# Kernel tuning notes

Measured on AMD Instinct MI355X. Metric: run time of the kernel, lower is better.

The kernel has to match this reference:

```python
import jax, jax.numpy as jnp
import numpy as np

HIDDEN = 768
FF = 3072
N_HEADS = 12
HEAD = HIDDEN // N_HEADS
WIDTH = 512  # attention window (number of attended keys, causal)
B, S = 2, 4096
EPS = 1e-6


def _rotary_sincos(seq_len, dim):
    # GPT-J style: freqs per pair, each value repeated twice (interleaved)
    inv_freq = 1.0 / (10000.0 ** (np.arange(0, dim, 2, dtype=np.float32) / dim))
    t = np.arange(seq_len, dtype=np.float32)
    ang = np.einsum('s,d->sd', t, inv_freq)              # [S, dim/2]
    ang = np.repeat(ang, 2, axis=-1)                     # [S, dim]
    return jnp.asarray(np.sin(ang))[:, None, :], jnp.asarray(np.cos(ang))[:, None, :]


def setup_inputs() -> dict:
    key = jax.random.key(0)
    ks = jax.random.split(key, 4)
    x = jax.random.normal(ks[0], (B, S, HIDDEN), dtype=jnp.float32)
    sin, cos = _rotary_sincos(S, HEAD)                   # [S,1,HEAD] each
    W_in = jax.random.normal(ks[1], (HIDDEN, 3 * HIDDEN + FF), dtype=jnp.float32) / np.sqrt(HIDDEN)
    b_in = jnp.zeros((3 * HIDDEN + FF,), dtype=jnp.float32)
    W_out = jax.random.normal(ks[2], (HIDDEN + FF, HIDDEN), dtype=jnp.float32) / np.sqrt(HIDDEN + FF)
    b_out = jnp.zeros((HIDDEN,), dtype=jnp.float32)
    w_norm = jnp.ones((HIDDEN,), dtype=jnp.float32)
    return {"x": x, "sin": sin, "cos": cos, "w_norm": w_norm,
            "W_in": W_in, "b_in": b_in, "W_out": W_out, "b_out": b_out}


def _rotate_every_two(x):
    x1 = x[..., ::2]
    x2 = x[..., 1::2]
    return jnp.stack((-x2, x1), axis=-1).reshape(x.shape)


def _apply_rope(x, sin, cos):
    # x: [B,S,H,hd]; sin/cos: [S,1,hd] -> broadcast as [1,S,1,hd]
    sin = sin[None]
    cos = cos[None]
    return x * cos + _rotate_every_two(x) * sin


def _windowed_attention(q, k, v, width):
    # q,k,v: [B,S,H,hd]; causal local attention: key j valid iff 0 <= i-j < width
    b, s, h, d = q.shape
    wb = width  # block size == window; each query block attends blocks (b-1, b)
    nb = s // wb
    scale = 1.0 / np.sqrt(d)
    qb = q.reshape(b, nb, wb, h, d)
    kp = jnp.pad(k, ((0, 0), (wb, 0), (0, 0), (0, 0))).reshape(b, nb + 1, wb, h, d)
    vp = jnp.pad(v, ((0, 0), (wb, 0), (0, 0), (0, 0))).reshape(b, nb + 1, wb, h, d)
    kb = jnp.concatenate([kp[:, :-1], kp[:, 1:]], axis=2)   # [B,nb,2wb,H,hd]
    vb = jnp.concatenate([vp[:, :-1], vp[:, 1:]], axis=2)
    scores = jnp.einsum('bnqhd,bnkhd->bnhqk', qb, kb) * scale
    qi = jnp.arange(wb)
    ki = jnp.arange(2 * wb)
    bi = jnp.arange(nb)
    diff = wb + qi[:, None] - ki[None, :]                    # i - j per block
    base = (diff >= 0) & (diff < width)                      # [wb, 2wb]
    valid_j = (bi[:, None, None] >= 1) | (ki[None, None, :] >= wb)  # j >= 0
    mask = base[None] & valid_j                              # [nb, wb, 2wb]
    neg = jnp.finfo(scores.dtype).min
    scores = jnp.where(mask[None, :, None], scores, neg)
    p = jax.nn.softmax(scores, axis=-1)
    out = jnp.einsum('bnhqk,bnkhd->bnqhd', p, vb)
    return out.reshape(b, s, h * d)


def reference(x, sin, cos, w_norm, W_in, b_in, W_out, b_out):
    # RMSNorm
    ms = jnp.mean(x * x, axis=-1, keepdims=True)
    xn = x * jax.lax.rsqrt(ms + EPS) * w_norm
    # fused QKV + FF projection
    t = xn @ W_in + b_in                                     # [B,S,3*HIDDEN+FF]
    ff = t[:, :, -FF:]
    qkv = t[:, :, :-FF].reshape(x.shape[0], x.shape[1], 3, N_HEADS, HEAD)
    q = _apply_rope(qkv[:, :, 0], sin, cos)
    k = _apply_rope(qkv[:, :, 1], sin, cos)
    v = qkv[:, :, 2]
    attn = _windowed_attention(q, k, v, WIDTH)               # [B,S,HIDDEN]
    ff = jax.nn.gelu(ff, approximate=False)
    combined = jnp.concatenate((attn, ff), axis=-1)          # [B,S,HIDDEN+FF]
    return combined @ W_out + b_out
```

## Files before the change

kernel.cpp:

```cpp
#include <hip/hip_runtime.h>
#include <hip/hip_bf16.h>

typedef short bf16x8 __attribute__((ext_vector_type(8)));
typedef float f32x4 __attribute__((ext_vector_type(4)));

#define LOG2E 1.4426950408889634f
#define QKV_E ((size_t)24*4096*64)

__device__ __forceinline__ float bfu2f(unsigned short u) {
  unsigned v = ((unsigned)u) << 16;
  return __builtin_bit_cast(float, v);
}
__device__ __forceinline__ unsigned short f2bfu(float f) {
  unsigned u = __builtin_bit_cast(unsigned, f);
  u += 0x7fffu + ((u >> 16) & 1u);
  return (unsigned short)(u >> 16);
}
__device__ __forceinline__ unsigned packbf2(float lo, float hi) {
  return (unsigned)f2bfu(lo) | ((unsigned)f2bfu(hi) << 16);
}
__device__ __forceinline__ float gelu_f(float v) {
  float a = fabsf(v) * 0.70710678118654752f;
  float t = 1.0f / (1.0f + 0.3275911f * a);
  float poly = ((((1.061405429f * t - 1.453152027f) * t + 1.421413741f) * t
                 - 0.284496736f) * t + 0.254829592f) * t;
  float erfa = 1.0f - poly * __expf(-a * a);
  float erfv = v >= 0.0f ? erfa : -erfa;
  return 0.5f * v * (1.0f + erfv);
}
__device__ __forceinline__ void gl_lds16(const ushort* g, ushort* l) {
  __builtin_amdgcn_global_load_lds(
      (const __attribute__((address_space(1))) unsigned int*)(const void*)g,
      (__attribute__((address_space(3))) unsigned int*)(void*)l, 16, 0, 0);
}
#define WAIT_VM8  asm volatile("s_waitcnt vmcnt(8)" ::: "memory")
#define WAIT_VM2  asm volatile("s_waitcnt vmcnt(2)" ::: "memory")
#define WAIT_VM0  asm volatile("s_waitcnt vmcnt(0)" ::: "memory")
#define WAIT_LGKM asm volatile("s_waitcnt lgkmcnt(0)" ::: "memory")
#define BAR       __builtin_amdgcn_s_barrier()

__global__ __launch_bounds__(256) void rmsnorm_k(const float* __restrict__ x,
    const float* __restrict__ w, ushort* __restrict__ xn) {
  int row = blockIdx.x, t = threadIdx.x;
  const float* xr = x + (size_t)row * 768;
  float v0 = xr[t], v1 = xr[t + 256], v2 = xr[t + 512];
  float ss = v0 * v0 + v1 * v1 + v2 * v2;
#pragma unroll
  for (int m = 32; m >= 1; m >>= 1) ss += __shfl_xor(ss, m, 64);
  __shared__ float part[4];
  if ((t & 63) == 0) part[t >> 6] = ss;
  __syncthreads();
  float tot = part[0] + part[1] + part[2] + part[3];
  float rr = rsqrtf(tot * (1.0f / 768.0f) + 1e-6f);
  ushort* xo = xn + (size_t)row * 768;
  xo[t]       = f2bfu(v0 * rr * w[t]);
  xo[t + 256] = f2bfu(v1 * rr * w[t + 256]);
  xo[t + 512] = f2bfu(v2 * rr * w[t + 512]);
}

__global__ __launch_bounds__(256) void tcvt_k(const float* __restrict__ in,
    ushort* __restrict__ out, int R, int C) {
  __shared__ float tile[32][33];
  int c0 = blockIdx.x * 32, r0 = blockIdx.y * 32;
  int t = threadIdx.x;
  int j = t & 31, i0 = t >> 5;
#pragma unroll
  for (int i = i0; i < 32; i += 8) tile[i][j] = in[(size_t)(r0 + i) * C + c0 + j];
  __syncthreads();
#pragma unroll
  for (int i = i0; i < 32; i += 8) out[(size_t)(c0 + i) * R + r0 + j] = f2bfu(tile[j][i]);
}

__global__ __launch_bounds__(512, 2) void gemm1_k(const ushort* __restrict__ A,
    const ushort* __restrict__ Bt, const float* __restrict__ bias,
    const float* __restrict__ sn, const float* __restrict__ cs,
    ushort* __restrict__ qbuf, ushort* __restrict__ kbuf,
    ushort* __restrict__ vt, ushort* __restrict__ comb) {
  __shared__ __align__(16) ushort lds[2][32768];
  const int t = threadIdx.x, lane = t & 63, w = t >> 6;
  const int wm = w >> 2, wn = w & 3;
  const int g = lane >> 4, q15 = lane & 15;
  int bid = blockIdx.x;
  int xcd = bid & 7, local = bid >> 3;
  int grp = local / 28, r28 = local % 28;
  int bx = grp * 7 + r28 % 7;
  int by = xcd * 4 + r28 / 7;
  const int mBase = by * 256, nBase = bx * 256;

  const int schk = ((t & 7) ^ ((t >> 3) & 7)) * 8;
  const ushort* gA = A  + (size_t)(mBase + (t >> 3)) * 768 + schk;
  const ushort* gB = Bt + (size_t)(nBase + (t >> 3)) * 768 + schk;
  const int dstBase = w * 512;

  f32x4 acc[8][4];
  f32x4 z = {0.f, 0.f, 0.f, 0.f};
#pragma unroll
  for (int mi = 0; mi < 8; ++mi)
#pragma unroll
    for (int nj = 0; nj < 4; ++nj) acc[mi][nj] = z;

#pragma unroll
  for (int rd = 0; rd < 4; ++rd) {
    gl_lds16(gB + rd * 49152, &lds[0][16384 + rd * 4096 + dstBase]);
    gl_lds16(gA + rd * 49152, &lds[0][rd * 4096 + dstBase]);
  }
  WAIT_VM0;
  BAR;

#pragma unroll 1
  for (int kt = 0; kt < 12; ++kt) {
    const int cur = kt & 1;
    const ushort* As = &lds[cur][0];
    const ushort* Bs = &lds[cur][16384];
    ushort* nb = &lds[1 - cur][0];
    bf16x8 bff[4];
#pragma unroll
    for (int p = 0; p < 4; ++p) {
      if (kt < 11) {
        const int k1 = (kt + 1) * 64;
        if (p == 0) {
          gl_lds16(gB + k1,               nb + 16384 + dstBase);
          gl_lds16(gB + 49152 + k1,       nb + 16384 + 4096 + dstBase);
        } else if (p == 1) {
          gl_lds16(gB + 2 * 49152 + k1,   nb + 16384 + 2 * 4096 + dstBase);
          gl_lds16(gB + 3 * 49152 + k1,   nb + 16384 + 3 * 4096 + dstBase);
        } else if (p == 2) {
          gl_lds16(gA + k1,               nb + dstBase);
          gl_lds16(gA + 2 * 49152 + k1,   nb + 2 * 4096 + dstBase);
        } else {
          gl_lds16(gA + 49152 + k1,       nb + 4096 + dstBase);
          gl_lds16(gA + 3 * 49152 + k1,   nb + 3 * 4096 + dstBase);
        }
      }
      const int kk = p >> 1, mih = p & 1;
      const int slot = ((kk * 4 + g) ^ (q15 & 7)) << 3;
      if (mih == 0) {
#pragma unroll
        for (int nj = 0; nj < 4; ++nj)
          bff[nj] = *(const bf16x8*)(Bs + (wn * 64 + nj * 16 + q15) * 64 + slot);
      }
      bf16x8 af[4];
#pragma unroll
      for (int i = 0; i < 4; ++i)
        af[i] = *(const bf16x8*)(As + (wm * 128 + (mih * 4 + i) * 16 + q15) * 64 + slot);
      BAR;
      WAIT_LGKM;
      __builtin_amdgcn_sched_barrier(0);
      __builtin_amdgcn_s_setprio(1);
#pragma unroll
      for (int i = 0; i < 4; ++i)
#pragma unroll
        for (int nj = 0; nj < 4; ++nj)
          acc[mih * 4 + i][nj] = __builtin_amdgcn_mfma_f32_16x16x32_bf16(
              bff[nj], af[i], acc[mih * 4 + i][nj], 0, 0, 0);
      __builtin_amdgcn_s_setprio(0);
      if (kt < 11) { WAIT_VM2; } else { WAIT_VM0; }
      BAR;
    }
  }

  const int colB = nBase + wn * 64;
  const bool isff = (colB >= 2304);
  const int region = colB / 768;
#pragma unroll
  for (int mi = 0; mi < 8; ++mi) {
    int row = mBase + wm * 128 + mi * 16 + q15;
    int b = row >> 12, s = row & 4095;
#pragma unroll
    for (int nj = 0; nj < 4; ++nj) {
      int col = colB + nj * 16 + g * 4;
      f32x4 v = acc[mi][nj] + *(const f32x4*)(bias + col);
      if (isff) {
        ushort4 o;
        o.x = f2bfu(gelu_f(v[0]));
        o.y = f2bfu(gelu_f(v[1]));
        o.z = f2bfu(gelu_f(v[2]));
        o.w = f2bfu(gelu_f(v[3]));
        *(ushort4*)(comb + (size_t)row * 3840 + (col - 1536)) = o;
      } else {
        int rem = col - region * 768;
        int h = rem >> 6, d0 = rem & 63;
        if (region == 2) {
          int l = s & 127;
          int pnn = l >> 4, pg = (l >> 2) & 3, pr = l & 3;
          int sp = (s & ~127) | (((pnn >> 1) * 4 + pg) * 8 + (pnn & 1) * 4 + pr);
          size_t vb = (size_t)((b * 12 + h) * 64 + d0) * 4096 + sp;
          vt[vb]          = f2bfu(v[0]);
          vt[vb + 4096]   = f2bfu(v[1]);
          vt[vb + 2*4096] = f2bfu(v[2]);
          vt[vb + 3*4096] = f2bfu(v[3]);
        } else {
          f32x4 sv = *(const f32x4*)(sn + (s << 6) + d0);
          f32x4 cv = *(const f32x4*)(cs + (s << 6) + d0);
          float o0 = v[0] * cv[0] - v[1] * sv[0];
          float o1 = v[1] * cv[0] + v[0] * sv[0];
          float o2 = v[2] * cv[2] - v[3] * sv[2];
          float o3 = v[3] * cv[2] + v[2] * sv[2];
          ushort4 o;
          if (region == 0) {
            o.x = f2bfu(o0 * 0.125f); o.y = f2bfu(o1 * 0.125f);
            o.z = f2bfu(o2 * 0.125f); o.w = f2bfu(o3 * 0.125f);
            *(ushort4*)(qbuf + ((size_t)((b * 12 + h) * 4096 + s)) * 64 + d0) = o;
          } else {
            o.x = f2bfu(o0); o.y = f2bfu(o1); o.z = f2bfu(o2); o.w = f2bfu(o3);
            *(ushort4*)(kbuf + ((size_t)((b * 12 + h) * 4096 + s)) * 64 + d0) = o;
          }
        }
      }
    }
  }
}

__global__ __launch_bounds__(256, 2) void gemm2_k(const ushort* __restrict__ A,
    const ushort* __restrict__ Bt, const float* __restrict__ bias,
    float* __restrict__ out) {
  __shared__ __align__(16) ushort lds[2][2][128 * 64];
  const int t = threadIdx.x, lane = t & 63, w = t >> 6;
  const int wr = w >> 1, wc = w & 1;
  int bid = blockIdx.x;
  int xcd = bid & 7, local = bid >> 3;
  int g = local / 4, r4 = local % 4;
  int bx = (g % 3) * 2 + (r4 & 1);
  int by = xcd * 8 + (g / 3) * 2 + (r4 >> 1);
  const int mBase = by * 128, nBase = bx * 128;

  size_t gA[4], gB[4];
  int ldst[4];
#pragma unroll
  for (int j = 0; j < 4; ++j) {
    int row = w * 32 + j * 8 + (lane >> 3);
    int gc = ((lane & 7) ^ (lane >> 3)) * 8;
    gA[j] = (size_t)(mBase + row) * 3840 + gc;
    gB[j] = (size_t)(nBase + row) * 3840 + gc;
    ldst[j] = (w * 32 + j * 8) * 64;
  }

  f32x4 acc[4][4];
  f32x4 z = {0.f, 0.f, 0.f, 0.f};
#pragma unroll
  for (int m = 0; m < 4; ++m)
#pragma unroll
    for (int nn = 0; nn < 4; ++nn) acc[m][nn] = z;

#pragma unroll
  for (int j = 0; j < 4; ++j) {
    gl_lds16(A + gA[j], &lds[0][0][0] + ldst[j]);
    gl_lds16(Bt + gB[j], &lds[0][1][0] + ldst[j]);
  }

#pragma unroll 1
  for (int kt = 0; kt < 60; ++kt) {
    const int cur = kt & 1;
    if (kt < 59) {
      int k0 = (kt + 1) * 64;
#pragma unroll
      for (int j = 0; j < 4; ++j) {
        gl_lds16(A + gA[j] + k0, &lds[1 - cur][0][0] + ldst[j]);
        gl_lds16(Bt + gB[j] + k0, &lds[1 - cur][1][0] + ldst[j]);
      }
      WAIT_VM8;
    } else {
      WAIT_VM0;
    }
    BAR;
    const ushort* As = &lds[cur][0][0];
    const ushort* Bs = &lds[cur][1][0];
#pragma unroll
    for (int kk = 0; kk < 2; ++kk) {
      bf16x8 af[4], bff[4];
#pragma unroll
      for (int m = 0; m < 4; ++m) {
        int row = wr * 64 + m * 16 + (lane & 15);
        int slot = (kk * 4 + (lane >> 4)) ^ (lane & 7);
        af[m] = *(const bf16x8*)(As + row * 64 + slot * 8);
      }
#pragma unroll
      for (int nn = 0; nn < 4; ++nn) {
        int row = wc * 64 + nn * 16 + (lane & 15);
        int slot = (kk * 4 + (lane >> 4)) ^ (lane & 7);
        bff[nn] = *(const bf16x8*)(Bs + row * 64 + slot * 8);
      }
#pragma unroll
      for (int m = 0; m < 4; ++m)
#pragma unroll
        for (int nn = 0; nn < 4; ++nn)
          acc[m][nn] = __builtin_amdgcn_mfma_f32_16x16x32_bf16(bff[nn], af[m], acc[m][nn], 0, 0, 0);
    }
    WAIT_LGKM;
    BAR;
  }

#pragma unroll
  for (int m = 0; m < 4; ++m) {
    int row = mBase + wr * 64 + m * 16 + (lane & 15);
#pragma unroll
    for (int nn = 0; nn < 4; ++nn) {
      int col = nBase + wc * 64 + nn * 16 + ((lane >> 4) << 2);
      f32x4 v = acc[m][nn] + *(const f32x4*)(bias + col);
      *(f32x4*)(out + (size_t)row * 768 + col) = v;
    }
  }
}

__global__ __launch_bounds__(256, 2) void attn_k(const ushort* __restrict__ qb,
    const ushort* __restrict__ kb, const ushort* __restrict__ vt,
    ushort* __restrict__ comb) {
  __shared__ __align__(16) ushort KS[2][128 * 64];
  __shared__ __align__(16) ushort VS[2][64 * 128];
  int bid = blockIdx.x;
  int nb = (bid & 7) * 96 + (bid >> 3);
  int qt = nb & 31, bh = nb >> 5;
  const int t = threadIdx.x, lane = t & 63, w = t >> 6;
  const int g = lane >> 4, q15 = lane & 15;
  const int qlo = qt * 128;
  const size_t base = (size_t)bh * 4096 * 64;

  size_t kSrc[4], vSrc[4];
  int dstOff[4];
#pragma unroll
  for (int j = 0; j < 4; ++j) {
    int ck = (w * 4 + j) * 64 + lane;
    int key = ck >> 3, sl = ck & 7;
    kSrc[j] = (size_t)key * 64 + ((sl ^ (key & 7)) << 3);
    int dd = ck >> 4, s16 = ck & 15;
    vSrc[j] = (size_t)dd * 4096 + ((s16 ^ (dd & 15)) << 3);
    dstOff[j] = (w * 4 + j) * 512;
  }

  bf16x8 qa[2][2];
#pragma unroll
  for (int m = 0; m < 2; ++m)
#pragma unroll
    for (int kk = 0; kk < 2; ++kk) {
      int row = qlo + w * 32 + m * 16 + q15;
      qa[m][kk] = *(const bf16x8*)(qb + base + (size_t)row * 64 + kk * 32 + g * 8);
    }

  f32x4 z = {0.f, 0.f, 0.f, 0.f};
  f32x4 o[2][4];
#pragma unroll
  for (int m = 0; m < 2; ++m)
#pragma unroll
    for (int df = 0; df < 4; ++df) o[m][df] = z;
  float m_run[2] = {-1e30f, -1e30f}, l_run[2] = {0.f, 0.f};

  const int t0 = qt >= 4 ? qt - 4 : 0;
  const int nt = qt - t0 + 1;
  {
    int k0 = t0 * 128;
#pragma unroll
    for (int j = 0; j < 4; ++j) {
      gl_lds16(kb + base + (size_t)k0 * 64 + kSrc[j], &KS[0][0] + dstOff[j]);
      gl_lds16(vt + base + k0 + vSrc[j], &VS[0][0] + dstOff[j]);
    }
  }

  const int qrow0 = qlo + w * 32 + q15;
#pragma unroll 1
  for (int it = 0; it < nt; ++it) {
    const int kt = t0 + it, k0 = kt * 128, cur = it & 1;
    if (it + 1 < nt) {
      int k1 = k0 + 128;
#pragma unroll
      for (int j = 0; j < 4; ++j) {
        gl_lds16(kb + base + (size_t)k1 * 64 + kSrc[j], &KS[1 - cur][0] + dstOff[j]);
        gl_lds16(vt + base + k1 + vSrc[j], &VS[1 - cur][0] + dstOff[j]);
      }
      WAIT_VM8;
    } else {
      WAIT_VM0;
    }
    BAR;
    f32x4 s[2][8];
#pragma unroll
    for (int m = 0; m < 2; ++m)
#pragma unroll
      for (int nn = 0; nn < 8; ++nn) s[m][nn] = z;
#pragma unroll
    for (int kk = 0; kk < 2; ++kk) {
      bf16x8 kf[8];
#pragma unroll
      for (int nn = 0; nn < 8; ++nn) {
        int row = nn * 16 + q15;
        int slot = (kk * 4 + g) ^ (q15 & 7);
        kf[nn] = *(const bf16x8*)(&KS[cur][0] + row * 64 + slot * 8);
      }
#pragma unroll
      for (int m = 0; m < 2; ++m)
#pragma unroll
        for (int nn = 0; nn < 8; ++nn)
          s[m][nn] = __builtin_amdgcn_mfma_f32_16x16x32_bf16(kf[nn], qa[m][kk], s[m][nn], 0, 0, 0);
    }
    if (kt == qt) {
#pragma unroll
      for (int m = 0; m < 2; ++m) {
        int ql = qrow0 + m * 16 - k0;
#pragma unroll
        for (int nn = 0; nn < 8; ++nn)
#pragma unroll
          for (int r = 0; r < 4; ++r)
            if (nn * 16 + g * 4 + r > ql) s[m][nn][r] = -3e38f;
      }
    } else if (kt == qt - 4) {
#pragma unroll
      for (int m = 0; m < 2; ++m) {
        int ql = qrow0 + m * 16 - k0;
#pragma unroll
        for (int nn = 0; nn < 8; ++nn)
#pragma unroll
          for (int r = 0; r < 4; ++r)
            if (ql - (nn * 16 + g * 4 + r) >= 512) s[m][nn][r] = -3e38f;
      }
    }
    float mx[2];
    bool need = false;
#pragma unroll
    for (int m = 0; m < 2; ++m) {
      float v = s[m][0][0];
#pragma unroll
      for (int nn = 0; nn < 8; ++nn)
#pragma unroll
        for (int r = 0; r < 4; ++r) v = fmaxf(v, s[m][nn][r]);
      v = fmaxf(v, __shfl_xor(v, 16, 64));
      v = fmaxf(v, __shfl_xor(v, 32, 64));
      mx[m] = v;
      need |= (v > m_run[m] + 8.f);
    }
    if (__any(need)) {
#pragma unroll
      for (int m = 0; m < 2; ++m) {
        float mn = fmaxf(m_run[m], mx[m]);
        float sc = exp2f((m_run[m] - mn) * LOG2E);
        m_run[m] = mn;
        l_run[m] *= sc;
#pragma unroll
        for (int df = 0; df < 4; ++df) o[m][df] *= sc;
      }
    }
#pragma unroll
    for (int m = 0; m < 2; ++m) {
      float mr = m_run[m];
      float ls = 0.f;
#pragma unroll
      for (int nn = 0; nn < 8; ++nn)
#pragma unroll
        for (int r = 0; r < 4; ++r) {
          float p = exp2f((s[m][nn][r] - mr) * LOG2E);
          s[m][nn][r] = p;
          ls += p;
        }
      ls += __shfl_xor(ls, 16, 64);
      ls += __shfl_xor(ls, 32, 64);
      l_run[m] += ls;
    }
#pragma unroll
    for (int kk2 = 0; kk2 < 4; ++kk2) {
      bf16x8 pa[2];
#pragma unroll
      for (int m = 0; m < 2; ++m) {
        int4 pi4;
        pi4.x = (int)packbf2(s[m][2*kk2][0],   s[m][2*kk2][1]);
        pi4.y = (int)packbf2(s[m][2*kk2][2],   s[m][2*kk2][3]);
        pi4.z = (int)packbf2(s[m][2*kk2+1][0], s[m][2*kk2+1][1]);
        pi4.w = (int)packbf2(s[m][2*kk2+1][2], s[m][2*kk2+1][3]);
        pa[m] = __builtin_bit_cast(bf16x8, pi4);
      }
#pragma unroll
      for (int df = 0; df < 4; ++df) {
        int row = df * 16 + q15;
        int slot = (kk2 * 4 + g) ^ q15;
        bf16x8 vf = *(const bf16x8*)(&VS[cur][0] + row * 128 + slot * 8);
#pragma unroll
        for (int m = 0; m < 2; ++m)
          o[m][df] = __builtin_amdgcn_mfma_f32_16x16x32_bf16(vf, pa[m], o[m][df], 0, 0, 0);
      }
    }
    WAIT_LGKM;
    BAR;
  }

  int b = bh / 12, h = bh % 12;
#pragma unroll
  for (int m = 0; m < 2; ++m) {
    float inv = 1.0f / l_run[m];
    int row = qrow0 + m * 16;
#pragma unroll
    for (int df = 0; df < 4; ++df) {
      ushort4 ov;
      ov.x = f2bfu(o[m][df][0] * inv);
      ov.y = f2bfu(o[m][df][1] * inv);
      ov.z = f2bfu(o[m][df][2] * inv);
      ov.w = f2bfu(o[m][df][3] * inv);
      *(ushort4*)(comb + (size_t)(b * 4096 + row) * 3840 + h * 64 + df * 16 + g * 4) = ov;
    }
  }
}

extern "C" void kernel_launch(void* const* d_in, const int* in_sizes, int n_in,
                              void* d_out, int out_size, void* d_ws, size_t ws_size,
                              hipStream_t stream) {
  (void)in_sizes; (void)n_in; (void)out_size; (void)ws_size;
  const float* x      = (const float*)d_in[0];
  const float* sin_t  = (const float*)d_in[1];
  const float* cos_t  = (const float*)d_in[2];
  const float* w_norm = (const float*)d_in[3];
  const float* W_in   = (const float*)d_in[4];
  const float* b_in   = (const float*)d_in[5];
  const float* W_out  = (const float*)d_in[6];
  const float* b_out  = (const float*)d_in[7];
  float* out = (float*)d_out;

  const size_t XN_E  = (size_t)8192 * 768;
  ushort* xn      = (ushort*)d_ws;
  ushort* qbuf    = xn + XN_E;
  ushort* kbuf    = qbuf + QKV_E;
  ushort* vt      = kbuf + QKV_E;
  ushort* w_in_t  = vt + QKV_E;
  ushort* w_out_t = w_in_t + (size_t)5376 * 768;
  ushort* comb    = w_out_t + (size_t)768 * 3840;

  rmsnorm_k<<<dim3(8192), dim3(256), 0, stream>>>(x, w_norm, xn);
  tcvt_k<<<dim3(5376 / 32, 768 / 32), dim3(256), 0, stream>>>(W_in, w_in_t, 768, 5376);
  tcvt_k<<<dim3(768 / 32, 3840 / 32), dim3(256), 0, stream>>>(W_out, w_out_t, 3840, 768);
  gemm1_k<<<dim3(672), dim3(512), 0, stream>>>(xn, w_in_t, b_in, sin_t, cos_t,
                                               qbuf, kbuf, vt, comb);
  attn_k<<<dim3(768), dim3(256), 0, stream>>>(qbuf, kbuf, vt, comb);
  gemm2_k<<<dim3(384), dim3(256), 0, stream>>>(comb, w_out_t, b_out, out);
}
```

Baseline: 239.4 us.

## Split-K gemm2 across two warp groups and simplify gemm1 pipeline

gemm2 now runs 512 threads per block, and each half of the block handles one half of the K dimension. The two partial accumulators are summed through LDS before the bias add and store, which doubles the waves per output tile to improve latency hiding. In exchange, gemm2 loses its double-buffered prefetch: every K step does a load followed by two __syncthreads with no overlap. gemm1's main loop is also restructured from four interleaved sub-phases, each with its own barriers and setprio, into a single prefetch-then-compute step per K tile with one wait and barrier.

```diff
diff --git a/kernel.cpp b/kernel.cpp
--- a/kernel.cpp
+++ b/kernel.cpp
@@ -34,7 +34,6 @@
       (__attribute__((address_space(3))) unsigned int*)(void*)l, 16, 0, 0);
 }
 #define WAIT_VM8  asm volatile("s_waitcnt vmcnt(8)" ::: "memory")
-#define WAIT_VM2  asm volatile("s_waitcnt vmcnt(2)" ::: "memory")
 #define WAIT_VM0  asm volatile("s_waitcnt vmcnt(0)" ::: "memory")
 #define WAIT_LGKM asm volatile("s_waitcnt lgkmcnt(0)" ::: "memory")
 #define BAR       __builtin_amdgcn_s_barrier()
@@ -101,62 +100,51 @@
 
 #pragma unroll
   for (int rd = 0; rd < 4; ++rd) {
+    gl_lds16(gA + rd * 49152, &lds[0][rd * 4096 + dstBase]);
     gl_lds16(gB + rd * 49152, &lds[0][16384 + rd * 4096 + dstBase]);
-    gl_lds16(gA + rd * 49152, &lds[0][rd * 4096 + dstBase]);
-  }
-  WAIT_VM0;
-  BAR;
+  }
 
 #pragma unroll 1
   for (int kt = 0; kt < 12; ++kt) {
     const int cur = kt & 1;
+    if (kt < 11) {
+      const int k1 = (kt + 1) * 64;
+      ushort* nb = &lds[1 - cur][0];
+#pragma unroll
+      for (int rd = 0; rd < 4; ++rd) {
+        gl_lds16(gA + rd * 49152 + k1, nb + rd * 4096 + dstBase);
+        gl_lds16(gB + rd * 49152 + k1, nb + 16384 + rd * 4096 + dstBase);
+      }
+      WAIT_VM8;
+    } else {
+      WAIT_VM0;
+    }
+    BAR;
     const ushort* As = &lds[cur][0];
     const ushort* Bs = &lds[cur][16384];
-    ushort* nb = &lds[1 - cur][0];
-    bf16x8 bff[4];
-#pragma unroll
-    for (int p = 0; p < 4; ++p) {
-      if (kt < 11) {
-        const int k1 = (kt + 1) * 64;
-        if (p == 0) {
-          gl_lds16(gB + k1,               nb + 16384 + dstBase);
-          gl_lds16(gB + 49152 + k1,       nb + 16384 + 4096 + dstBase);
-        } else if (p == 1) {
-          gl_lds16(gB + 2 * 49152 + k1,   nb + 16384 + 2 * 4096 + dstBase);
-          gl_lds16(gB + 3 * 49152 + k1,   nb + 16384 + 3 * 4096 + dstBase);
-        } else if (p == 2) {
-          gl_lds16(gA + k1,               nb + dstBase);
-          gl_lds16(gA + 2 * 49152 + k1,   nb + 2 * 4096 + dstBase);
-        } else {
-          gl_lds16(gA + 49152 + k1,       nb + 4096 + dstBase);
-          gl_lds16(gA + 3 * 49152 + k1,   nb + 3 * 4096 + dstBase);
-        }
-      }
-      const int kk = p >> 1, mih = p & 1;
+#pragma unroll
+    for (int kk = 0; kk < 2; ++kk) {
       const int slot = ((kk * 4 + g) ^ (q15 & 7)) << 3;
-      if (mih == 0) {
-#pragma unroll
-        for (int nj = 0; nj < 4; ++nj)
-          bff[nj] = *(const bf16x8*)(Bs + (wn * 64 + nj * 16 + q15) * 64 + slot);
-      }
-      bf16x8 af[4];
-#pragma unroll
-      for (int i = 0; i < 4; ++i)
-        af[i] = *(const bf16x8*)(As + (wm * 128 + (mih * 4 + i) * 16 + q15) * 64 + slot);
-      BAR;
-      WAIT_LGKM;
-      __builtin_amdgcn_sched_barrier(0);
-      __builtin_amdgcn_s_setprio(1);
-#pragma unroll
-      for (int i = 0; i < 4; ++i)
-#pragma unroll
-        for (int nj = 0; nj < 4; ++nj)
-          acc[mih * 4 + i][nj] = __builtin_amdgcn_mfma_f32_16x16x32_bf16(
-              bff[nj], af[i], acc[mih * 4 + i][nj], 0, 0, 0);
-      __builtin_amdgcn_s_setprio(0);
-      if (kt < 11) { WAIT_VM2; } else { WAIT_VM0; }
-      BAR;
-    }
+      bf16x8 bff[4];
+#pragma unroll
+      for (int nj = 0; nj < 4; ++nj)
+        bff[nj] = *(const bf16x8*)(Bs + (wn * 64 + nj * 16 + q15) * 64 + slot);
+#pragma unroll
+      for (int mih = 0; mih < 2; ++mih) {
+        bf16x8 af[4];
+#pragma unroll
+        for (int i = 0; i < 4; ++i)
+          af[i] = *(const bf16x8*)(As + (wm * 128 + (mih * 4 + i) * 16 + q15) * 64 + slot);
+#pragma unroll
+        for (int i = 0; i < 4; ++i)
+#pragma unroll
+          for (int nj = 0; nj < 4; ++nj)
+            acc[mih * 4 + i][nj] = __builtin_amdgcn_mfma_f32_16x16x32_bf16(
+                bff[nj], af[i], acc[mih * 4 + i][nj], 0, 0, 0);
+      }
+    }
+    WAIT_LGKM;
+    BAR;
   }
 
   const int colB = nBase + wn * 64;
@@ -211,28 +199,31 @@
   }
 }
 
-__global__ __launch_bounds__(256, 2) void gemm2_k(const ushort* __restrict__ A,
+__global__ __launch_bounds__(512, 2) void gemm2_k(const ushort* __restrict__ A,
     const ushort* __restrict__ Bt, const float* __restrict__ bias,
     float* __restrict__ out) {
   __shared__ __align__(16) ushort lds[2][2][128 * 64];
-  const int t = threadIdx.x, lane = t & 63, w = t >> 6;
-  const int wr = w >> 1, wc = w & 1;
+  const int t = threadIdx.x;
+  const int grp = t >> 8, tl = t & 255;
+  const int lane = tl & 63, w4 = tl >> 6;
+  const int wr = w4 >> 1, wc = w4 & 1;
   int bid = blockIdx.x;
   int xcd = bid & 7, local = bid >> 3;
   int g = local / 4, r4 = local % 4;
   int bx = (g % 3) * 2 + (r4 & 1);
   int by = xcd * 8 + (g / 3) * 2 + (r4 >> 1);
   const int mBase = by * 128, nBase = bx * 128;
+  const int kOff = grp * 1920;
 
   size_t gA[4], gB[4];
   int ldst[4];
 #pragma unroll
   for (int j = 0; j < 4; ++j) {
-    int row = w * 32 + j * 8 + (lane >> 3);
+    int row = w4 * 32 + j * 8 + (lane >> 3);
     int gc = ((lane & 7) ^ (lane >> 3)) * 8;
-    gA[j] = (size_t)(mBase + row) * 3840 + gc;
-    gB[j] = (size_t)(nBase + row) * 3840 + gc;
-    ldst[j] = (w * 32 + j * 8) * 64;
+    gA[j] = (size_t)(mBase + row) * 3840 + kOff + gc;
+    gB[j] = (size_t)(nBase + row) * 3840 + kOff + gc;
+    ldst[j] = (w4 * 32 + j * 8) * 64;
   }
 
   f32x4 acc[4][4];
@@ -242,29 +233,16 @@
 #pragma unroll
     for (int nn = 0; nn < 4; ++nn) acc[m][nn] = z;
 
-#pragma unroll
-  for (int j = 0; j < 4; ++j) {
-    gl_lds16(A + gA[j], &lds[0][0][0] + ldst[j]);
-    gl_lds16(Bt + gB[j], &lds[0][1][0] + ldst[j]);
-  }
-
 #pragma unroll 1
-  for (int kt = 0; kt < 60; ++kt) {
-    const int cur = kt & 1;
-    if (kt < 59) {
-      int k0 = (kt + 1) * 64;
-#pragma unroll
-      for (int j = 0; j < 4; ++j) {
-        gl_lds16(A + gA[j] + k0, &lds[1 - cur][0][0] + ldst[j]);
-        gl_lds16(Bt + gB[j] + k0, &lds[1 - cur][1][0] + ldst[j]);
-      }
-      WAIT_VM8;
-    } else {
-      WAIT_VM0;
-    }
-    BAR;
-    const ushort* As = &lds[cur][0][0];
-    const ushort* Bs = &lds[cur][1][0];
+  for (int kt = 0; kt < 30; ++kt) {
+    const int k0 = kt * 64;
+    __syncthreads();
+#pragma unroll
+    for (int j = 0; j < 4; ++j) {
+      gl_lds16(A + gA[j] + k0, &lds[grp][0][0] + ldst[j]);
+      gl_lds16(Bt + gB[j] + k0, &lds[grp][1][0] + ldst[j]);
+    }
+    __syncthreads();
 #pragma unroll
     for (int kk = 0; kk < 2; ++kk) {
       bf16x8 af[4], bff[4];
@@ -272,13 +250,13 @@
       for (int m = 0; m < 4; ++m) {
         int row = wr * 64 + m * 16 + (lane & 15);
         int slot = (kk * 4 + (lane >> 4)) ^ (lane & 7);
-        af[m] = *(const bf16x8*)(As + row * 64 + slot * 8);
+        af[m] = *(const bf16x8*)(&lds[grp][0][0] + row * 64 + slot * 8);
       }
 #pragma unroll
       for (int nn = 0; nn < 4; ++nn) {
         int row = wc * 64 + nn * 16 + (lane & 15);
         int slot = (kk * 4 + (lane >> 4)) ^ (lane & 7);
-        bff[nn] = *(const bf16x8*)(Bs + row * 64 + slot * 8);
+        bff[nn] = *(const bf16x8*)(&lds[grp][1][0] + row * 64 + slot * 8);
       }
 #pragma unroll
       for (int m = 0; m < 4; ++m)
@@ -286,18 +264,32 @@
         for (int nn = 0; nn < 4; ++nn)
           acc[m][nn] = __builtin_amdgcn_mfma_f32_16x16x32_bf16(bff[nn], af[m], acc[m][nn], 0, 0, 0);
     }
-    WAIT_LGKM;
-    BAR;
-  }
-
-#pragma unroll
-  for (int m = 0; m < 4; ++m) {
-    int row = mBase + wr * 64 + m * 16 + (lane & 15);
-#pragma unroll
-    for (int nn = 0; nn < 4; ++nn) {
-      int col = nBase + wc * 64 + nn * 16 + ((lane >> 4) << 2);
-      f32x4 v = acc[m][nn] + *(const f32x4*)(bias + col);
-      *(f32x4*)(out + (size_t)row * 768 + col) = v;
+  }
+
+  f32x4* sc = (f32x4*)&lds[0][0][0];
+#pragma unroll
+  for (int h = 0; h < 2; ++h) {
+    __syncthreads();
+    if (grp == 1) {
+#pragma unroll
+      for (int m = 0; m < 2; ++m)
+#pragma unroll
+        for (int nn = 0; nn < 4; ++nn)
+          sc[(size_t)tl * 8 + m * 4 + nn] = acc[2 * h + m][nn];
+    }
+    __syncthreads();
+    if (grp == 0) {
+#pragma unroll
+      for (int m = 0; m < 2; ++m) {
+        int row = mBase + wr * 64 + (2 * h + m) * 16 + (lane & 15);
+#pragma unroll
+        for (int nn = 0; nn < 4; ++nn) {
+          int col = nBase + wc * 64 + nn * 16 + ((lane >> 4) << 2);
+          f32x4 v = acc[2 * h + m][nn] + sc[(size_t)tl * 8 + m * 4 + nn]
+                  + *(const f32x4*)(bias + col);
+          *(f32x4*)(out + (size_t)row * 768 + col) = v;
+        }
+      }
     }
   }
 }
@@ -525,5 +517,5 @@
   gemm1_k<<<dim3(672), dim3(512), 0, stream>>>(xn, w_in_t, b_in, sin_t, cos_t,
                                                qbuf, kbuf, vt, comb);
   attn_k<<<dim3(768), dim3(256), 0, stream>>>(qbuf, kbuf, vt, comb);
-  gemm2_k<<<dim3(384), dim3(256), 0, stream>>>(comb, w_out_t, b_out, out);
-}
+  gemm2_k<<<dim3(384), dim3(512), 0, stream>>>(comb, w_out_t, b_out, out);
+}
```

New measurement: 232.3 us. -3.0%, faster.
